# Performance work log

Measured on AMD Instinct MI355X. Metric: run time of the kernel, lower is better.

## Reference

```python
import jax, jax.numpy as jnp
import numpy as np

N_NODES = 50000
N_EDGES = 250000
T_POOL = 4
C = 300


def setup_inputs() -> dict:
    key = jax.random.key(0)
    ks = jax.random.split(key, 7)
    x = jax.random.normal(ks[0], (N_NODES, T_POOL, C), dtype=jnp.float32)
    # edges guaranteed non-self-loop (so remove_self_loops is a no-op)
    row = jax.random.randint(ks[1], (N_EDGES,), 0, N_NODES, dtype=jnp.int32)
    off = jax.random.randint(ks[2], (N_EDGES,), 1, N_NODES, dtype=jnp.int32)
    col = (row + off) % N_NODES
    edge_index = jnp.stack([row, col], axis=0)
    W1 = jax.random.normal(ks[3], (300, C), dtype=jnp.float32) * 0.05
    b1 = jax.random.normal(ks[4], (300,), dtype=jnp.float32) * 0.05
    W2 = jax.random.normal(ks[5], (300, 300), dtype=jnp.float32) * 0.05
    b2 = jax.random.normal(ks[6], (300,), dtype=jnp.float32) * 0.05
    return {"x": x, "edge_index": edge_index, "W1": W1, "b1": b1, "W2": W2, "b2": b2}


def reference(x, edge_index, W1, b1, W2, b2):
    N = x.shape[0]
    row, col = edge_index[0], edge_index[1]
    # add self loops (input edges contain no self loops)
    sl = jnp.arange(N, dtype=row.dtype)
    row = jnp.concatenate([row, sl])
    col = jnp.concatenate([col, sl])
    # symmetric sqrt-degree norm, degree computed on source (row)
    deg = jax.ops.segment_sum(jnp.ones(row.shape[0], dtype=x.dtype), row, num_segments=N)
    dis = deg ** -0.5  # [N]

    def prop(h):  # out[i] = dis[i] * sum_{e: col_e=i} dis[row_e] * h[row_e]
        msg = (dis[:, None] * h)[row]  # [E+N, d]
        return dis[:, None] * jax.ops.segment_sum(msg, col, num_segments=N)

    # layer 1: linear -> mean pool over dim 1 -> propagate -> leaky_relu
    h = jnp.mean(jnp.einsum('ntc,oc->nto', x, W1) + b1, axis=1)  # [N, 300]
    h = jax.nn.leaky_relu(prop(h), negative_slope=0.01)
    # layer 2: linear -> propagate
    h2 = h @ W2.T + b2  # [N, out]
    return prop(h2)
```

## Files before the change

### kernel.cpp

```cpp
#include <hip/hip_runtime.h>

typedef __attribute__((ext_vector_type(8))) short bf16x8;
typedef __attribute__((ext_vector_type(4))) float f32x4;

__device__ __forceinline__ unsigned short f2bf(float f) {
    union { float f; unsigned u; } v; v.f = f;
    unsigned r = (v.u + 0x7FFFu + ((v.u >> 16) & 1u)) >> 16;
    return (unsigned short)r;
}
__device__ __forceinline__ unsigned pack2bf(float a, float b) {
    return (unsigned)f2bf(a) | ((unsigned)f2bf(b) << 16);
}
__device__ __forceinline__ float bflo(unsigned u) { union { unsigned u; float f; } v; v.u = u << 16; return v.f; }
__device__ __forceinline__ float bfhi(unsigned u) { union { unsigned u; float f; } v; v.u = u & 0xffff0000u; return v.f; }

__global__ void pool_kernel(const float* __restrict__ x, unsigned short* __restrict__ xm,
                            int N, int Mpad) {
    int tid = blockIdx.x * 256 + threadIdx.x;
    if (tid >= Mpad * 40) return;
    int n = tid / 40, k8 = tid % 40;
    int k = k8 * 8;
    float v[8] = {0.f,0.f,0.f,0.f,0.f,0.f,0.f,0.f};
    if (n < N && k < 300) {
        const float* xp = x + (size_t)n * 1200 + k;
        #pragma unroll
        for (int t = 0; t < 4; ++t) {
            const float4 lo = *(const float4*)(xp + t * 300);
            v[0] += lo.x; v[1] += lo.y; v[2] += lo.z; v[3] += lo.w;
            if (k + 4 < 300) {
                const float4 hi = *(const float4*)(xp + t * 300 + 4);
                v[4] += hi.x; v[5] += hi.y; v[6] += hi.z; v[7] += hi.w;
            }
        }
    }
    union { unsigned short u[8]; bf16x8 vec; } p;
    #pragma unroll
    for (int j = 0; j < 8; ++j) p.u[j] = f2bf(v[j] * 0.25f);
    *(bf16x8*)(xm + (size_t)tid * 8) = p.vec;
}

__global__ void setup_kernel(const float* __restrict__ W1, const float* __restrict__ b1,
                             const float* __restrict__ W2, const float* __restrict__ b2,
                             unsigned short* __restrict__ Ws1, unsigned short* __restrict__ Ws2,
                             float* __restrict__ bp1, float* __restrict__ bp2,
                             int* __restrict__ deg, int* __restrict__ cnt, int* __restrict__ cur, int N) {
    int tid = blockIdx.x * 256 + threadIdx.x;
    if (tid < N) { deg[tid] = 0; cnt[tid] = 0; cur[tid] = 0; }
    if (tid < 304 * 320) {
        int c = tid / 320, k = tid % 320;
        int ks = k / 32, kk = k % 32;
        int cp  = c * 4 + (kk >> 3);
        int cps = cp ^ (c & 7);
        int dst = ks * 9728 + cps * 8 + (kk & 7);
        bool in = (c < 300) && (k < 300);
        Ws1[dst] = f2bf(in ? W1[c * 300 + k] : 0.f);
        Ws2[dst] = f2bf(in ? W2[c * 300 + k] : 0.f);
        if (tid < 304) { bp1[tid] = tid < 300 ? b1[tid] : 0.f; bp2[tid] = tid < 300 ? b2[tid] : 0.f; }
    }
}

__global__ void degcnt_kernel(const int* __restrict__ ei, int E,
                              int* __restrict__ deg, int* __restrict__ cnt) {
    int e = blockIdx.x * 256 + threadIdx.x;
    if (e >= E) return;
    atomicAdd(&deg[ei[e]], 1);
    atomicAdd(&cnt[ei[E + e]], 1);
}

__global__ void scanA_kernel(const int* __restrict__ cnt, int* __restrict__ bsum, int N) {
    __shared__ int sm[256];
    int i = blockIdx.x * 256 + threadIdx.x;
    sm[threadIdx.x] = (i < N) ? cnt[i] : 0;
    __syncthreads();
    for (int off = 128; off > 0; off >>= 1) {
        if (threadIdx.x < off) sm[threadIdx.x] += sm[threadIdx.x + off];
        __syncthreads();
    }
    if (threadIdx.x == 0) bsum[blockIdx.x] = sm[0];
}

__global__ void scanB_kernel(int* __restrict__ bsum, int nb, int* __restrict__ indptr, int N) {
    __shared__ int sm[256];
    int t = threadIdx.x;
    int v = (t < nb) ? bsum[t] : 0;
    sm[t] = v; __syncthreads();
    for (int off = 1; off < 256; off <<= 1) {
        int u = (t >= off) ? sm[t - off] : 0;
        __syncthreads();
        sm[t] += u;
        __syncthreads();
    }
    if (t < nb) bsum[t] = sm[t] - v;
    if (t == 255) indptr[N] = sm[255];
}

__global__ void scanC_kernel(const int* __restrict__ cnt, const int* __restrict__ bsum,
                             int* __restrict__ indptr, const int* __restrict__ deg,
                             float* __restrict__ dis, int N) {
    __shared__ int sm[256];
    int i = blockIdx.x * 256 + threadIdx.x;
    int c = (i < N) ? cnt[i] : 0;
    sm[threadIdx.x] = c; __syncthreads();
    for (int off = 1; off < 256; off <<= 1) {
        int u = (threadIdx.x >= off) ? sm[threadIdx.x - off] : 0;
        __syncthreads();
        sm[threadIdx.x] += u;
        __syncthreads();
    }
    if (i < N) {
        indptr[i] = bsum[blockIdx.x] + sm[threadIdx.x] - c;
        dis[i] = 1.0f / sqrtf((float)(deg[i] + 1));
    }
}

__global__ void fill_kernel(const int* __restrict__ ei, int E,
                            const int* __restrict__ indptr, int* __restrict__ cur,
                            int* __restrict__ csr) {
    int e = blockIdx.x * 256 + threadIdx.x;
    if (e >= E) return;
    int r = ei[e], c = ei[E + e];
    int pos = indptr[c] + atomicAdd(&cur[c], 1);
    csr[pos] = r;
}

__global__ __launch_bounds__(512, 4) void gemm_kernel(
    const unsigned short* __restrict__ A, const unsigned short* __restrict__ Ws,
    const float* __restrict__ bp, const float* __restrict__ dis,
    unsigned short* __restrict__ g, int N)
{
    __shared__ __align__(16) unsigned short lds[2][9728];
    const int t = threadIdx.x;
    const int lane = t & 63;
    const int wave = t >> 6;
    const int l15 = lane & 15, lhi = lane >> 4;
    const int rowBase = blockIdx.x * 128 + wave * 16;

    const unsigned short* Ap = A + (size_t)(rowBase + l15) * 320 + lhi * 8;
    const uint4* Wsrc = (const uint4*)Ws;

    const int rb16 = (l15 * 4 + lhi) ^ (l15 & 7);

    for (int grp = wave; grp < 19; grp += 8)
        __builtin_amdgcn_global_load_lds(
            (const __attribute__((address_space(1))) unsigned*)(Wsrc + grp * 64 + lane),
            (__attribute__((address_space(3))) unsigned*)(&lds[0][0] + grp * 512),
            16, 0, 0);

    bf16x8 a0 = *(const bf16x8*)(Ap);
    bf16x8 a1 = *(const bf16x8*)(Ap + 32);

    f32x4 acc[19];
    #pragma unroll
    for (int i = 0; i < 19; ++i) acc[i] = (f32x4){0.f,0.f,0.f,0.f};

    #pragma unroll
    for (int ks = 0; ks < 10; ++ks) {
        __syncthreads();
        if (ks < 9) {
            const uint4* s = Wsrc + (ks + 1) * 1216;
            unsigned short* d = &lds[(ks + 1) & 1][0];
            for (int grp = wave; grp < 19; grp += 8)
                __builtin_amdgcn_global_load_lds(
                    (const __attribute__((address_space(1))) unsigned*)(s + grp * 64 + lane),
                    (__attribute__((address_space(3))) unsigned*)(d + grp * 512),
                    16, 0, 0);
        }
        const unsigned short* lb = &lds[ks & 1][0] + rb16 * 8;
        #pragma unroll
        for (int cf = 0; cf < 19; ++cf) {
            bf16x8 b = *(const bf16x8*)(lb + cf * 512);
            acc[cf] = __builtin_amdgcn_mfma_f32_16x16x32_bf16(a0, b, acc[cf], 0, 0, 0);
        }
        a0 = a1;
        if (ks < 8) a1 = *(const bf16x8*)(Ap + (ks + 2) * 32);
    }

    const int n0 = rowBase + lhi * 4;
    float dd[4];
    #pragma unroll
    for (int r = 0; r < 4; ++r) dd[r] = (n0 + r < N) ? dis[n0 + r] : 0.f;
    #pragma unroll
    for (int cf = 0; cf < 19; ++cf) {
        int o = cf * 16 + l15;
        if (o < 300) {
            float bo = bp[o];
            #pragma unroll
            for (int r = 0; r < 4; ++r)
                if (n0 + r < N) g[(size_t)(n0 + r) * 320 + o] = f2bf(dd[r] * (acc[cf][r] + bo));
        }
    }
}

template<int MODE>
__global__ void prop_kernel(const unsigned short* __restrict__ g, const int* __restrict__ indptr,
                            const int* __restrict__ csr, const float* __restrict__ dis,
                            void* __restrict__ outp, int N, int Mpad) {
    int wave = threadIdx.x >> 6;
    int lane = threadIdx.x & 63;
    int n = blockIdx.x * 4 + wave;
    if (n >= (MODE ? Mpad : N)) return;
    const bool act = lane < 38;
    float aL[4] = {0.f,0.f,0.f,0.f}, aH[4] = {0.f,0.f,0.f,0.f};
    if (n < N) {
        if (act) {
            uint4 u = *((const uint4*)(g + (size_t)n * 320) + lane);
            aL[0] = bflo(u.x); aH[0] = bfhi(u.x);
            aL[1] = bflo(u.y); aH[1] = bfhi(u.y);
            aL[2] = bflo(u.z); aH[2] = bfhi(u.z);
            aL[3] = bflo(u.w); aH[3] = bfhi(u.w);
        }
        int beg = indptr[n], end = indptr[n + 1];
        int j = beg;
        for (; j + 4 <= end; j += 4) {
            int s0 = csr[j], s1 = csr[j+1], s2 = csr[j+2], s3 = csr[j+3];
            const uint4* p0 = (const uint4*)(g + (size_t)s0 * 320) + lane;
            const uint4* p1 = (const uint4*)(g + (size_t)s1 * 320) + lane;
            const uint4* p2 = (const uint4*)(g + (size_t)s2 * 320) + lane;
            const uint4* p3 = (const uint4*)(g + (size_t)s3 * 320) + lane;
            if (act) {
                uint4 u0 = *p0, u1 = *p1, u2 = *p2, u3 = *p3;
                aL[0] += bflo(u0.x) + bflo(u1.x) + bflo(u2.x) + bflo(u3.x);
                aH[0] += bfhi(u0.x) + bfhi(u1.x) + bfhi(u2.x) + bfhi(u3.x);
                aL[1] += bflo(u0.y) + bflo(u1.y) + bflo(u2.y) + bflo(u3.y);
                aH[1] += bfhi(u0.y) + bfhi(u1.y) + bfhi(u2.y) + bfhi(u3.y);
                aL[2] += bflo(u0.z) + bflo(u1.z) + bflo(u2.z) + bflo(u3.z);
                aH[2] += bfhi(u0.z) + bfhi(u1.z) + bfhi(u2.z) + bfhi(u3.z);
                aL[3] += bflo(u0.w) + bflo(u1.w) + bflo(u2.w) + bflo(u3.w);
                aH[3] += bfhi(u0.w) + bfhi(u1.w) + bfhi(u2.w) + bfhi(u3.w);
            }
        }
        for (; j < end; ++j) {
            const uint4* ps = (const uint4*)(g + (size_t)csr[j] * 320) + lane;
            if (act) {
                uint4 u = *ps;
                aL[0] += bflo(u.x); aH[0] += bfhi(u.x);
                aL[1] += bflo(u.y); aH[1] += bfhi(u.y);
                aL[2] += bflo(u.z); aH[2] += bfhi(u.z);
                aL[3] += bflo(u.w); aH[3] += bfhi(u.w);
            }
        }
        float dn = dis[n];
        #pragma unroll
        for (int i = 0; i < 4; ++i) { aL[i] *= dn; aH[i] *= dn; }
    }
    if (MODE == 0) {
        float* out = (float*)outp + (size_t)n * 300 + lane * 8;
        if (lane < 37) {
            float4 f0 = {aL[0], aH[0], aL[1], aH[1]};
            float4 f1 = {aL[2], aH[2], aL[3], aH[3]};
            *(float4*)out = f0;
            *(float4*)(out + 4) = f1;
        } else if (lane == 37) {
            float4 f0 = {aL[0], aH[0], aL[1], aH[1]};
            *(float4*)out = f0;
        }
    } else {
        uint4* h = (uint4*)((unsigned*)outp + (size_t)n * 160) + lane;
        if (lane < 40) {
            uint4 w = {0u, 0u, 0u, 0u};
            if (act) {
                float vL, vH;
                vL = aL[0]; vL = vL > 0.f ? vL : 0.01f * vL;
                vH = aH[0]; vH = vH > 0.f ? vH : 0.01f * vH;
                w.x = pack2bf(vL, vH);
                vL = aL[1]; vL = vL > 0.f ? vL : 0.01f * vL;
                vH = aH[1]; vH = vH > 0.f ? vH : 0.01f * vH;
                w.y = pack2bf(vL, vH);
                vL = aL[2]; vL = vL > 0.f ? vL : 0.01f * vL;
                vH = aH[2]; vH = vH > 0.f ? vH : 0.01f * vH;
                w.z = pack2bf(vL, vH);
                vL = aL[3]; vL = vL > 0.f ? vL : 0.01f * vL;
                vH = aH[3]; vH = vH > 0.f ? vH : 0.01f * vH;
                w.w = pack2bf(vL, vH);
                if (lane == 37) { w.z = 0u; w.w = 0u; }
            }
            *h = w;
        }
    }
}

extern "C" void kernel_launch(void* const* d_in, const int* in_sizes, int n_in,
                              void* d_out, int out_size, void* d_ws, size_t ws_size,
                              hipStream_t stream) {
    const float* x  = (const float*)d_in[0];
    const int*   ei = (const int*)d_in[1];
    const float* W1 = (const float*)d_in[2];
    const float* b1 = (const float*)d_in[3];
    const float* W2 = (const float*)d_in[4];
    const float* b2 = (const float*)d_in[5];
    float* out = (float*)d_out;

    const int N = in_sizes[0] / 1200;
    const int E = in_sizes[1] / 2;
    const int Mpad = ((N + 127) / 128) * 128;
    const int NB = (N + 255) / 256;

    char* p = (char*)d_ws;
    auto carve = [&](size_t bytes) -> char* {
        char* r = p; p += (bytes + 255) & ~(size_t)255; return r;
    };
    unsigned short* xm   = (unsigned short*)carve((size_t)Mpad * 320 * 2);
    unsigned short* g1   = (unsigned short*)carve((size_t)Mpad * 320 * 2);
    unsigned short* hb   = (unsigned short*)carve((size_t)Mpad * 320 * 2);
    unsigned short* g2   = (unsigned short*)carve((size_t)Mpad * 320 * 2);
    float* dis           = (float*)carve((size_t)N * 4);
    int* deg             = (int*)carve((size_t)N * 4);
    int* cnt             = (int*)carve((size_t)N * 4);
    int* indptr          = (int*)carve((size_t)(N + 1) * 4);
    int* cur             = (int*)carve((size_t)N * 4);
    int* csr             = (int*)carve((size_t)E * 4);
    int* bsum            = (int*)carve(256 * 4);
    unsigned short* Ws1  = (unsigned short*)carve(304 * 320 * 2);
    unsigned short* Ws2  = (unsigned short*)carve(304 * 320 * 2);
    float* bp1           = (float*)carve(304 * 4);
    float* bp2           = (float*)carve(304 * 4);

    setup_kernel <<<(304 * 320 + 255) / 256, 256, 0, stream>>>(W1, b1, W2, b2, Ws1, Ws2, bp1, bp2,
                                                               deg, cnt, cur, N);
    pool_kernel  <<<(Mpad * 40 + 255) / 256, 256, 0, stream>>>(x, xm, N, Mpad);
    degcnt_kernel<<<(E + 255) / 256, 256, 0, stream>>>(ei, E, deg, cnt);
    scanA_kernel <<<NB, 256, 0, stream>>>(cnt, bsum, N);
    scanB_kernel <<<1, 256, 0, stream>>>(bsum, NB, indptr, N);
    scanC_kernel <<<NB, 256, 0, stream>>>(cnt, bsum, indptr, deg, dis, N);
    fill_kernel  <<<(E + 255) / 256, 256, 0, stream>>>(ei, E, indptr, cur, csr);

    gemm_kernel  <<<Mpad / 128, 512, 0, stream>>>(xm, Ws1, bp1, dis, g1, N);
    prop_kernel<1><<<Mpad / 4, 256, 0, stream>>>(g1, indptr, csr, dis, hb, N, Mpad);
    gemm_kernel  <<<Mpad / 128, 512, 0, stream>>>(hb, Ws2, bp2, dis, g2, N);
    prop_kernel<0><<<(N + 3) / 4, 256, 0, stream>>>(g2, indptr, csr, dis, out, N, Mpad);
}
```

Measured before the change: 253.5 us.

## Replace three-pass scan with atomic bucket offsets and preload GEMM A fragments

The three-kernel prefix scan that built CSR row pointers is replaced by a single kernel. Each block does a local scan and reserves a contiguous range with one atomicAdd on a global counter, storing (start, count) pairs per node. This removes two kernel launches and the serial middle pass, but the CSR segments are no longer in node order, which may reduce locality in the propagation gathers. Separately, the GEMM now loads all ten A fragments up front and relaxes launch bounds to 2 blocks per CU, trading register pressure and occupancy for fewer in-loop global loads.

```diff
diff --git a/kernel.cpp b/kernel.cpp
--- a/kernel.cpp
+++ b/kernel.cpp
@@ -43,8 +43,10 @@
                              const float* __restrict__ W2, const float* __restrict__ b2,
                              unsigned short* __restrict__ Ws1, unsigned short* __restrict__ Ws2,
                              float* __restrict__ bp1, float* __restrict__ bp2,
-                             int* __restrict__ deg, int* __restrict__ cnt, int* __restrict__ cur, int N) {
+                             int* __restrict__ deg, int* __restrict__ cnt, int* __restrict__ cur,
+                             int* __restrict__ total, int N) {
     int tid = blockIdx.x * 256 + threadIdx.x;
+    if (tid == 0) *total = 0;
     if (tid < N) { deg[tid] = 0; cnt[tid] = 0; cur[tid] = 0; }
     if (tid < 304 * 320) {
         int c = tid / 320, k = tid % 320;
@@ -67,37 +69,11 @@
     atomicAdd(&cnt[ei[E + e]], 1);
 }
 
-__global__ void scanA_kernel(const int* __restrict__ cnt, int* __restrict__ bsum, int N) {
+__global__ void bucket_kernel(const int* __restrict__ cnt, const int* __restrict__ deg,
+                              int2* __restrict__ bkt, float* __restrict__ dis,
+                              int* __restrict__ total, int N) {
     __shared__ int sm[256];
-    int i = blockIdx.x * 256 + threadIdx.x;
-    sm[threadIdx.x] = (i < N) ? cnt[i] : 0;
-    __syncthreads();
-    for (int off = 128; off > 0; off >>= 1) {
-        if (threadIdx.x < off) sm[threadIdx.x] += sm[threadIdx.x + off];
-        __syncthreads();
-    }
-    if (threadIdx.x == 0) bsum[blockIdx.x] = sm[0];
-}
-
-__global__ void scanB_kernel(int* __restrict__ bsum, int nb, int* __restrict__ indptr, int N) {
-    __shared__ int sm[256];
-    int t = threadIdx.x;
-    int v = (t < nb) ? bsum[t] : 0;
-    sm[t] = v; __syncthreads();
-    for (int off = 1; off < 256; off <<= 1) {
-        int u = (t >= off) ? sm[t - off] : 0;
-        __syncthreads();
-        sm[t] += u;
-        __syncthreads();
-    }
-    if (t < nb) bsum[t] = sm[t] - v;
-    if (t == 255) indptr[N] = sm[255];
-}
-
-__global__ void scanC_kernel(const int* __restrict__ cnt, const int* __restrict__ bsum,
-                             int* __restrict__ indptr, const int* __restrict__ deg,
-                             float* __restrict__ dis, int N) {
-    __shared__ int sm[256];
+    __shared__ int sbase;
     int i = blockIdx.x * 256 + threadIdx.x;
     int c = (i < N) ? cnt[i] : 0;
     sm[threadIdx.x] = c; __syncthreads();
@@ -107,23 +83,25 @@
         sm[threadIdx.x] += u;
         __syncthreads();
     }
+    if (threadIdx.x == 255) sbase = atomicAdd(total, sm[255]);
+    __syncthreads();
     if (i < N) {
-        indptr[i] = bsum[blockIdx.x] + sm[threadIdx.x] - c;
+        bkt[i] = make_int2(sbase + sm[threadIdx.x] - c, c);
         dis[i] = 1.0f / sqrtf((float)(deg[i] + 1));
     }
 }
 
 __global__ void fill_kernel(const int* __restrict__ ei, int E,
-                            const int* __restrict__ indptr, int* __restrict__ cur,
+                            const int2* __restrict__ bkt, int* __restrict__ cur,
                             int* __restrict__ csr) {
     int e = blockIdx.x * 256 + threadIdx.x;
     if (e >= E) return;
     int r = ei[e], c = ei[E + e];
-    int pos = indptr[c] + atomicAdd(&cur[c], 1);
+    int pos = bkt[c].x + atomicAdd(&cur[c], 1);
     csr[pos] = r;
 }
 
-__global__ __launch_bounds__(512, 4) void gemm_kernel(
+__global__ __launch_bounds__(512, 2) void gemm_kernel(
     const unsigned short* __restrict__ A, const unsigned short* __restrict__ Ws,
     const float* __restrict__ bp, const float* __restrict__ dis,
     unsigned short* __restrict__ g, int N)
@@ -146,8 +124,9 @@
             (__attribute__((address_space(3))) unsigned*)(&lds[0][0] + grp * 512),
             16, 0, 0);
 
-    bf16x8 a0 = *(const bf16x8*)(Ap);
-    bf16x8 a1 = *(const bf16x8*)(Ap + 32);
+    bf16x8 a[10];
+    #pragma unroll
+    for (int ks = 0; ks < 10; ++ks) a[ks] = *(const bf16x8*)(Ap + ks * 32);
 
     f32x4 acc[19];
     #pragma unroll
@@ -169,10 +148,8 @@
         #pragma unroll
         for (int cf = 0; cf < 19; ++cf) {
             bf16x8 b = *(const bf16x8*)(lb + cf * 512);
-            acc[cf] = __builtin_amdgcn_mfma_f32_16x16x32_bf16(a0, b, acc[cf], 0, 0, 0);
-        }
-        a0 = a1;
-        if (ks < 8) a1 = *(const bf16x8*)(Ap + (ks + 2) * 32);
+            acc[cf] = __builtin_amdgcn_mfma_f32_16x16x32_bf16(a[ks], b, acc[cf], 0, 0, 0);
+        }
     }
 
     const int n0 = rowBase + lhi * 4;
@@ -192,7 +169,7 @@
 }
 
 template<int MODE>
-__global__ void prop_kernel(const unsigned short* __restrict__ g, const int* __restrict__ indptr,
+__global__ void prop_kernel(const unsigned short* __restrict__ g, const int2* __restrict__ bkt,
                             const int* __restrict__ csr, const float* __restrict__ dis,
                             void* __restrict__ outp, int N, int Mpad) {
     int wave = threadIdx.x >> 6;
@@ -209,7 +186,8 @@
             aL[2] = bflo(u.z); aH[2] = bfhi(u.z);
             aL[3] = bflo(u.w); aH[3] = bfhi(u.w);
         }
-        int beg = indptr[n], end = indptr[n + 1];
+        int2 bk = bkt[n];
+        int beg = bk.x, end = bk.x + bk.y;
         int j = beg;
         for (; j + 4 <= end; j += 4) {
             int s0 = csr[j], s1 = csr[j+1], s2 = csr[j+2], s3 = csr[j+3];
@@ -306,26 +284,24 @@
     float* dis           = (float*)carve((size_t)N * 4);
     int* deg             = (int*)carve((size_t)N * 4);
     int* cnt             = (int*)carve((size_t)N * 4);
-    int* indptr          = (int*)carve((size_t)(N + 1) * 4);
+    int2* bkt            = (int2*)carve((size_t)N * 8);
     int* cur             = (int*)carve((size_t)N * 4);
     int* csr             = (int*)carve((size_t)E * 4);
-    int* bsum            = (int*)carve(256 * 4);
+    int* total           = (int*)carve(256);
     unsigned short* Ws1  = (unsigned short*)carve(304 * 320 * 2);
     unsigned short* Ws2  = (unsigned short*)carve(304 * 320 * 2);
     float* bp1           = (float*)carve(304 * 4);
     float* bp2           = (float*)carve(304 * 4);
 
     setup_kernel <<<(304 * 320 + 255) / 256, 256, 0, stream>>>(W1, b1, W2, b2, Ws1, Ws2, bp1, bp2,
-                                                               deg, cnt, cur, N);
+                                                               deg, cnt, cur, total, N);
     pool_kernel  <<<(Mpad * 40 + 255) / 256, 256, 0, stream>>>(x, xm, N, Mpad);
     degcnt_kernel<<<(E + 255) / 256, 256, 0, stream>>>(ei, E, deg, cnt);
-    scanA_kernel <<<NB, 256, 0, stream>>>(cnt, bsum, N);
-    scanB_kernel <<<1, 256, 0, stream>>>(bsum, NB, indptr, N);
-    scanC_kernel <<<NB, 256, 0, stream>>>(cnt, bsum, indptr, deg, dis, N);
-    fill_kernel  <<<(E + 255) / 256, 256, 0, stream>>>(ei, E, indptr, cur, csr);
+    bucket_kernel<<<NB, 256, 0, stream>>>(cnt, deg, bkt, dis, total, N);
+    fill_kernel  <<<(E + 255) / 256, 256, 0, stream>>>(ei, E, bkt, cur, csr);
 
     gemm_kernel  <<<Mpad / 128, 512, 0, stream>>>(xm, Ws1, bp1, dis, g1, N);
-    prop_kernel<1><<<Mpad / 4, 256, 0, stream>>>(g1, indptr, csr, dis, hb, N, Mpad);
+    prop_kernel<1><<<Mpad / 4, 256, 0, stream>>>(g1, bkt, csr, dis, hb, N, Mpad);
     gemm_kernel  <<<Mpad / 128, 512, 0, stream>>>(hb, Ws2, bp2, dis, g2, N);
-    prop_kernel<0><<<(N + 3) / 4, 256, 0, stream>>>(g2, indptr, csr, dis, out, N, Mpad);
-}
+    prop_kernel<0><<<(N + 3) / 4, 256, 0, stream>>>(g2, bkt, csr, dis, out, N, Mpad);
+}
```

Result: slower. 267.6 us (+5.5%).
